# Performance work log

Hardware: AMD Instinct MI355X
Metric: run time of the kernel (lower is better)

Reference implementation:

```python
import jax, jax.numpy as jnp
import numpy as np

D = 256   # input_dim (also per-head dim)
H = 8     # num_heads
B = 32
S = 1024


def setup_inputs() -> dict:
    key = jax.random.key(0)
    ks = jax.random.split(key, 9)
    scale = 1.0 / np.sqrt(D)
    x = jax.random.normal(ks[0], (B, S, D), dtype=jnp.float32)
    Wk = jax.random.normal(ks[1], (D, D * H), dtype=jnp.float32) * scale
    bk = jnp.zeros((D * H,), dtype=jnp.float32)
    Wv = jax.random.normal(ks[2], (D, D * H), dtype=jnp.float32) * scale
    bv = jnp.zeros((D * H,), dtype=jnp.float32)
    query = jax.random.normal(ks[3], (H, D), dtype=jnp.float32)
    Wo = jax.random.normal(ks[4], (D * H, D), dtype=jnp.float32) / np.sqrt(D * H)
    bo = jnp.zeros((D,), dtype=jnp.float32)
    return {"x": x, "Wk": Wk, "bk": bk, "Wv": Wv, "bv": bv,
            "query": query, "Wo": Wo, "bo": bo}


def reference(x, Wk, bk, Wv, bv, query, Wo, bo):
    b, s, _ = x.shape
    # keys/values: [B, S, H, D]
    keys = (x @ Wk + bk).reshape(b, s, H, D)
    values = (x @ Wv + bv).reshape(b, s, H, D)
    # per-head single-query scores over sequence: [B, S, H]
    scores = jnp.einsum("bshd,hd->bsh", keys, query)
    attn = jax.nn.softmax(scores, axis=1)
    # attention-pooled values per head: [B, H, D] -> concat [B, H*D]
    pooled = jnp.einsum("bsh,bshd->bhd", attn, values).reshape(b, H * D)
    return pooled @ Wo + bo
```

## Files before the change

kernel.cpp:

```cpp
#include <hip/hip_runtime.h>

#define D 256
#define H 8
#define B 32
#define S 1024
#define SCH 32
#define SCS 32

#define OFF_QK   0
#define OFF_SB   2048
#define OFF_ML   2056
#define OFF_XWP  18440

__global__ void __launch_bounds__(256) k_prep(
        const float* __restrict__ Wk, const float* __restrict__ bk,
        const float* __restrict__ query, const float* __restrict__ bo,
        float* __restrict__ qk, float* __restrict__ sb,
        float* __restrict__ out) {
    __shared__ float red[256];
    const int h  = blockIdx.x >> 5;
    const int kc = blockIdx.x & 31;
    const int t  = threadIdx.x;
    const int kl = t >> 5;
    const int dq = t & 31;
    const int k  = kc * 8 + kl;
    const int d0 = dq * 8;
    const float* wrow = Wk + (size_t)k * (D * H) + h * D + d0;
    const float* qrow = query + h * D + d0;
    const float4 w0 = *(const float4*)(wrow);
    const float4 w1 = *(const float4*)(wrow + 4);
    const float4 q0 = *(const float4*)(qrow);
    const float4 q1 = *(const float4*)(qrow + 4);
    float acc = w0.x * q0.x + w0.y * q0.y + w0.z * q0.z + w0.w * q0.w
              + w1.x * q1.x + w1.y * q1.y + w1.z * q1.z + w1.w * q1.w;
    #pragma unroll
    for (int msk = 1; msk < 32; msk <<= 1) acc += __shfl_xor(acc, msk);
    if (dq == 0) qk[h * D + k] = acc;
    if (kc == 0) {
        red[t] = bk[h * D + t] * query[h * D + t];
        __syncthreads();
        for (int st = 128; st > 0; st >>= 1) {
            if (t < st) red[t] += red[t + st];
            __syncthreads();
        }
        if (t == 0) sb[h] = red[0];
    }
    if (h == 0) out[(size_t)kc * D + t] = bo[t];
}

__global__ void __launch_bounds__(256, 4) k_fused(
        const float* __restrict__ x, const float* __restrict__ qk,
        const float* __restrict__ sb, float* __restrict__ xwp,
        float2* __restrict__ mlbuf) {
    const int b  = blockIdx.x >> 5;
    const int c  = blockIdx.x & 31;
    const int s0 = c * SCS;
    const int t  = threadIdx.x;
    __shared__ float qkL[H * D];
    __shared__ float sbL[H];
    __shared__ float sc[SCS][H];
    {
        float4* q4 = (float4*)qkL;
        q4[t]       = ((const float4*)qk)[t];
        q4[t + 256] = ((const float4*)qk)[t + 256];
        if (t < H) sbL[t] = sb[t];
    }
    __syncthreads();

    {
        const int sl = t >> 3;
        const int dq = t & 7;
        const int d0 = dq * 32;
        const float* xrow = x + ((size_t)(b * S + s0 + sl)) * D + d0;
        float4 xr[8];
        #pragma unroll
        for (int j0 = 0; j0 < 8; j0++) {
            const int je = (j0 + dq) & 7;
            xr[j0] = *(const float4*)(xrow + je * 4);
        }
        float accA[H];
        #pragma unroll
        for (int hh = 0; hh < H; hh++) {
            const float* qb = &qkL[hh * D + d0];
            float a = 0.f;
            #pragma unroll
            for (int j0 = 0; j0 < 8; j0++) {
                const int je = (j0 + dq) & 7;
                const float4 qv = *(const float4*)(qb + je * 4);
                a += xr[j0].x * qv.x + xr[j0].y * qv.y
                   + xr[j0].z * qv.z + xr[j0].w * qv.w;
            }
            accA[hh] = a;
        }
        #pragma unroll
        for (int hh = 0; hh < H; hh++) {
            accA[hh] += __shfl_xor(accA[hh], 1);
            accA[hh] += __shfl_xor(accA[hh], 2);
            accA[hh] += __shfl_xor(accA[hh], 4);
        }
        if (dq == 0) {
            #pragma unroll
            for (int hh = 0; hh < H; hh++)
                sc[sl][hh] = accA[hh] + sbL[hh];
        }
    }
    __syncthreads();

    {
        const int hh = t >> 5;
        const int u  = t & 31;
        const float v = sc[u][hh];
        float m = v;
        #pragma unroll
        for (int msk = 1; msk < 32; msk <<= 1) m = fmaxf(m, __shfl_xor(m, msk));
        const float e = __expf(v - m);
        float sum = e;
        #pragma unroll
        for (int msk = 1; msk < 32; msk <<= 1) sum += __shfl_xor(sum, msk);
        sc[u][hh] = e;
        if (u == 0) mlbuf[((size_t)(b * H + hh)) * SCH + c] = make_float2(m, sum);
    }
    __syncthreads();

    {
        float acc2[H] = {};
        const float* xp = x + ((size_t)(b * S + s0)) * D + t;
        #pragma unroll 8
        for (int s = 0; s < SCS; s++) {
            const float xv = xp[(size_t)s * D];
            const float4 pa = *(const float4*)(&sc[s][0]);
            const float4 pb = *(const float4*)(&sc[s][4]);
            acc2[0] += pa.x * xv; acc2[1] += pa.y * xv;
            acc2[2] += pa.z * xv; acc2[3] += pa.w * xv;
            acc2[4] += pb.x * xv; acc2[5] += pb.y * xv;
            acc2[6] += pb.z * xv; acc2[7] += pb.w * xv;
        }
        #pragma unroll
        for (int hh = 0; hh < H; hh++)
            xwp[(((size_t)(b * H + hh)) * SCH + c) * D + t] = acc2[hh];
    }
}

__global__ void __launch_bounds__(256, 4) k_po(
        const float* __restrict__ xwp, const float2* __restrict__ mlbuf,
        const float* __restrict__ Wv, const float* __restrict__ bv,
        const float* __restrict__ Wo, float* __restrict__ out) {
    const int blk = blockIdx.x;
    const int dvh = blk & 1;
    const int bh  = blk >> 1;
    const int b = bh >> 3, h = bh & 7;
    const int t = threadIdx.x;
    __shared__ float scaleL[SCH];
    __shared__ float xwL[D];
    __shared__ float pp[256];
    __shared__ float pooledL[128];

    if (t < SCH) {
        const float2 ml = mlbuf[((size_t)(b * H + h)) * SCH + t];
        float M = ml.x;
        #pragma unroll
        for (int msk = 1; msk < 32; msk <<= 1) M = fmaxf(M, __shfl_xor(M, msk));
        const float p = __expf(ml.x - M);
        float L = ml.y * p;
        #pragma unroll
        for (int msk = 1; msk < 32; msk <<= 1) L += __shfl_xor(L, msk);
        scaleL[t] = p / L;
    }
    __syncthreads();
    {
        const float* xp = xwp + ((size_t)(b * H + h)) * SCH * D + t;
        float acc = 0.f;
        #pragma unroll 8
        for (int cc = 0; cc < SCH; cc++)
            acc += xp[(size_t)cc * D] * scaleL[cc];
        xwL[t] = acc;
    }
    __syncthreads();
    {
        const int kseg = t >> 7;
        const int dvl  = t & 127;
        const float* wp = Wv + (size_t)(kseg * 128) * (D * H) + h * D + dvh * 128 + dvl;
        float acc = 0.f;
        #pragma unroll 8
        for (int dd = 0; dd < 128; dd++)
            acc += xwL[kseg * 128 + dd] * wp[(size_t)dd * (D * H)];
        pp[t] = acc;
    }
    __syncthreads();
    if (t < 128) pooledL[t] = pp[t] + pp[t + 128] + bv[h * D + dvh * 128 + t];
    __syncthreads();
    {
        const float* wo = Wo + (size_t)(h * D + dvh * 128) * D + t;
        float acc = 0.f;
        #pragma unroll 8
        for (int dv = 0; dv < 128; dv++)
            acc += pooledL[dv] * wo[(size_t)dv * D];
        atomicAdd(out + (size_t)b * D + t, acc);
    }
}

extern "C" void kernel_launch(void* const* d_in, const int* in_sizes, int n_in,
                              void* d_out, int out_size, void* d_ws, size_t ws_size,
                              hipStream_t stream) {
    const float* x     = (const float*)d_in[0];
    const float* Wk    = (const float*)d_in[1];
    const float* bk    = (const float*)d_in[2];
    const float* Wv    = (const float*)d_in[3];
    const float* bv    = (const float*)d_in[4];
    const float* query = (const float*)d_in[5];
    const float* Wo    = (const float*)d_in[6];
    const float* bo    = (const float*)d_in[7];
    float* out = (float*)d_out;
    float* ws  = (float*)d_ws;

    float*  qk    = ws + OFF_QK;
    float*  sb    = ws + OFF_SB;
    float2* mlbuf = (float2*)(ws + OFF_ML);
    float*  xwp   = ws + OFF_XWP;

    k_prep<<<dim3(H * 32), dim3(256), 0, stream>>>(Wk, bk, query, bo, qk, sb, out);
    k_fused<<<dim3(B * SCH), dim3(256), 0, stream>>>(x, qk, sb, xwp, mlbuf);
    k_po<<<dim3(B * H * 2), dim3(256), 0, stream>>>(xwp, mlbuf, Wv, bv, Wo, out);
}
```

Before: 118.5 us.

## Stage x tile in LDS, drop softmax-invariant score bias, split k_po four ways

After: 129.6 us. +9.4%, slower.

```diff
diff --git a/kernel.cpp b/kernel.cpp
--- a/kernel.cpp
+++ b/kernel.cpp
@@ -6,18 +6,16 @@
 #define S 1024
 #define SCH 32
 #define SCS 32
+#define XPAD 4
 
 #define OFF_QK   0
-#define OFF_SB   2048
-#define OFF_ML   2056
-#define OFF_XWP  18440
+#define OFF_ML   2048
+#define OFF_XWP  18432
 
 __global__ void __launch_bounds__(256) k_prep(
-        const float* __restrict__ Wk, const float* __restrict__ bk,
-        const float* __restrict__ query, const float* __restrict__ bo,
-        float* __restrict__ qk, float* __restrict__ sb,
+        const float* __restrict__ Wk, const float* __restrict__ query,
+        const float* __restrict__ bo, float* __restrict__ qk,
         float* __restrict__ out) {
-    __shared__ float red[256];
     const int h  = blockIdx.x >> 5;
     const int kc = blockIdx.x & 31;
     const int t  = threadIdx.x;
@@ -36,37 +34,18 @@
     #pragma unroll
     for (int msk = 1; msk < 32; msk <<= 1) acc += __shfl_xor(acc, msk);
     if (dq == 0) qk[h * D + k] = acc;
-    if (kc == 0) {
-        red[t] = bk[h * D + t] * query[h * D + t];
-        __syncthreads();
-        for (int st = 128; st > 0; st >>= 1) {
-            if (t < st) red[t] += red[t + st];
-            __syncthreads();
-        }
-        if (t == 0) sb[h] = red[0];
-    }
     if (h == 0) out[(size_t)kc * D + t] = bo[t];
 }
 
 __global__ void __launch_bounds__(256, 4) k_fused(
         const float* __restrict__ x, const float* __restrict__ qk,
-        const float* __restrict__ sb, float* __restrict__ xwp,
-        float2* __restrict__ mlbuf) {
+        float* __restrict__ xwp, float2* __restrict__ mlbuf) {
     const int b  = blockIdx.x >> 5;
     const int c  = blockIdx.x & 31;
     const int s0 = c * SCS;
     const int t  = threadIdx.x;
-    __shared__ float qkL[H * D];
-    __shared__ float sbL[H];
+    __shared__ float xL[SCS][D + XPAD];
     __shared__ float sc[SCS][H];
-    {
-        float4* q4 = (float4*)qkL;
-        q4[t]       = ((const float4*)qk)[t];
-        q4[t + 256] = ((const float4*)qk)[t + 256];
-        if (t < H) sbL[t] = sb[t];
-    }
-    __syncthreads();
-
     {
         const int sl = t >> 3;
         const int dq = t & 7;
@@ -75,18 +54,17 @@
         float4 xr[8];
         #pragma unroll
         for (int j0 = 0; j0 < 8; j0++) {
-            const int je = (j0 + dq) & 7;
-            xr[j0] = *(const float4*)(xrow + je * 4);
+            xr[j0] = *(const float4*)(xrow + j0 * 4);
+            *(float4*)(&xL[sl][d0 + j0 * 4]) = xr[j0];
         }
         float accA[H];
         #pragma unroll
         for (int hh = 0; hh < H; hh++) {
-            const float* qb = &qkL[hh * D + d0];
+            const float* qb = qk + hh * D + d0;
             float a = 0.f;
             #pragma unroll
             for (int j0 = 0; j0 < 8; j0++) {
-                const int je = (j0 + dq) & 7;
-                const float4 qv = *(const float4*)(qb + je * 4);
+                const float4 qv = *(const float4*)(qb + j0 * 4);
                 a += xr[j0].x * qv.x + xr[j0].y * qv.y
                    + xr[j0].z * qv.z + xr[j0].w * qv.w;
             }
@@ -100,8 +78,7 @@
         }
         if (dq == 0) {
             #pragma unroll
-            for (int hh = 0; hh < H; hh++)
-                sc[sl][hh] = accA[hh] + sbL[hh];
+            for (int hh = 0; hh < H; hh++) sc[sl][hh] = accA[hh];
         }
     }
     __syncthreads();
@@ -124,10 +101,9 @@
 
     {
         float acc2[H] = {};
-        const float* xp = x + ((size_t)(b * S + s0)) * D + t;
         #pragma unroll 8
         for (int s = 0; s < SCS; s++) {
-            const float xv = xp[(size_t)s * D];
+            const float xv = xL[s][t];
             const float4 pa = *(const float4*)(&sc[s][0]);
             const float4 pb = *(const float4*)(&sc[s][4]);
             acc2[0] += pa.x * xv; acc2[1] += pa.y * xv;
@@ -146,14 +122,14 @@
         const float* __restrict__ Wv, const float* __restrict__ bv,
         const float* __restrict__ Wo, float* __restrict__ out) {
     const int blk = blockIdx.x;
-    const int dvh = blk & 1;
-    const int bh  = blk >> 1;
+    const int dvq = blk & 3;
+    const int bh  = blk >> 2;
     const int b = bh >> 3, h = bh & 7;
     const int t = threadIdx.x;
     __shared__ float scaleL[SCH];
     __shared__ float xwL[D];
     __shared__ float pp[256];
-    __shared__ float pooledL[128];
+    __shared__ float pooledL[64];
 
     if (t < SCH) {
         const float2 ml = mlbuf[((size_t)(b * H + h)) * SCH + t];
@@ -177,23 +153,25 @@
     }
     __syncthreads();
     {
-        const int kseg = t >> 7;
-        const int dvl  = t & 127;
-        const float* wp = Wv + (size_t)(kseg * 128) * (D * H) + h * D + dvh * 128 + dvl;
+        const int kseg = t >> 6;
+        const int dvl  = t & 63;
+        const float* wp = Wv + (size_t)(kseg * 64) * (D * H) + h * D + dvq * 64 + dvl;
         float acc = 0.f;
         #pragma unroll 8
-        for (int dd = 0; dd < 128; dd++)
-            acc += xwL[kseg * 128 + dd] * wp[(size_t)dd * (D * H)];
+        for (int dd = 0; dd < 64; dd++)
+            acc += xwL[kseg * 64 + dd] * wp[(size_t)dd * (D * H)];
         pp[t] = acc;
     }
     __syncthreads();
-    if (t < 128) pooledL[t] = pp[t] + pp[t + 128] + bv[h * D + dvh * 128 + t];
-    __syncthreads();
-    {
-        const float* wo = Wo + (size_t)(h * D + dvh * 128) * D + t;
+    if (t < 64)
+        pooledL[t] = pp[t] + pp[t + 64] + pp[t + 128] + pp[t + 192]
+                   + bv[h * D + dvq * 64 + t];
+    __syncthreads();
+    {
+        const float* wo = Wo + (size_t)(h * D + dvq * 64) * D + t;
         float acc = 0.f;
         #pragma unroll 8
-        for (int dv = 0; dv < 128; dv++)
+        for (int dv = 0; dv < 64; dv++)
             acc += pooledL[dv] * wo[(size_t)dv * D];
         atomicAdd(out + (size_t)b * D + t, acc);
     }
@@ -204,7 +182,6 @@
                               hipStream_t stream) {
     const float* x     = (const float*)d_in[0];
     const float* Wk    = (const float*)d_in[1];
-    const float* bk    = (const float*)d_in[2];
     const float* Wv    = (const float*)d_in[3];
     const float* bv    = (const float*)d_in[4];
     const float* query = (const float*)d_in[5];
@@ -214,11 +191,10 @@
     float* ws  = (float*)d_ws;
 
     float*  qk    = ws + OFF_QK;
-    float*  sb    = ws + OFF_SB;
     float2* mlbuf = (float2*)(ws + OFF_ML);
     float*  xwp   = ws + OFF_XWP;
 
-    k_prep<<<dim3(H * 32), dim3(256), 0, stream>>>(Wk, bk, query, bo, qk, sb, out);
-    k_fused<<<dim3(B * SCH), dim3(256), 0, stream>>>(x, qk, sb, xwp, mlbuf);
-    k_po<<<dim3(B * H * 2), dim3(256), 0, stream>>>(xwp, mlbuf, Wv, bv, Wo, out);
-}
+    k_prep<<<dim3(H * 32), dim3(256), 0, stream>>>(Wk, query, bo, qk, out);
+    k_fused<<<dim3(B * SCH), dim3(256), 0, stream>>>(x, qk, xwp, mlbuf);
+    k_po<<<dim3(B * H * 4), dim3(256), 0, stream>>>(xwp, mlbuf, Wv, bv, Wo, out);
+}
```
